# Performance work log

Hardware: AMD Instinct MI355X
Metric: run time of the kernel (lower is better)

## Reference

```python
import jax, jax.numpy as jnp
import numpy as np

B, N = 32, 512
NODE_F, EDGE_F = 64, 16
OUT = [64, 64, 64, 128]
TARGET = 16
DEGS = [1, 2, 3, 4]  # degree buckets (degree 0 filtered out, as in init_duvenaud)


def setup_inputs() -> dict:
    key = jax.random.key(0)
    ks = jax.random.split(key, 12)
    # adjacency: each node v connects to v+1..v+deg(v) (mod N), deg in {1..4}
    deg = jax.random.randint(ks[0], (B, N), 1, 5)
    off = jnp.arange(1, 5)                                   # (4,)
    cols = (jnp.arange(N)[:, None] + off[None, :]) % N       # (N,4)
    vals = (off[None, None, :] <= deg[:, :, None]).astype(jnp.float32)  # (B,N,4)
    g = jnp.zeros((B, N, N), jnp.float32).at[:, jnp.arange(N)[:, None], cols].set(vals)
    h_in = jax.random.normal(ks[1], (B, N, NODE_F), jnp.float32)
    e = jax.random.normal(ks[2], (B, N, N, EDGE_F), jnp.float32)
    # per-timestep, per-degree update matrices H_t: (n_deg, msg_in_t, out_t)
    ins = [NODE_F + EDGE_F, OUT[0] + EDGE_F, OUT[1] + EDGE_F]
    H0 = jax.random.normal(ks[3], (len(DEGS), ins[0], OUT[0]), jnp.float32)
    H1 = jax.random.normal(ks[4], (len(DEGS), ins[1], OUT[1]), jnp.float32)
    H2 = jax.random.normal(ks[5], (len(DEGS), ins[2], OUT[2]), jnp.float32)
    # readout matrices W_l for each of the 4 stored layers h^0..h^3
    layer_in = [NODE_F, OUT[0], OUT[1], OUT[2]]
    W0 = jax.random.normal(ks[6], (layer_in[0], OUT[3]), jnp.float32)
    W1 = jax.random.normal(ks[7], (layer_in[1], OUT[3]), jnp.float32)
    W2 = jax.random.normal(ks[8], (layer_in[2], OUT[3]), jnp.float32)
    W3 = jax.random.normal(ks[9], (layer_in[3], OUT[3]), jnp.float32)
    W_final = jax.random.normal(ks[10], (OUT[3], TARGET), jnp.float32) * 0.05
    b_final = jnp.zeros((TARGET,), jnp.float32)
    return {"g": g, "h_in": h_in, "e": e,
            "H0": H0, "H1": H1, "H2": H2,
            "W0": W0, "W1": W1, "W2": W2, "W3": W3,
            "W_final": W_final, "b_final": b_final}


def _step(g, e, h, H):
    # duvenaud message m_v = sum_w g[v,w] * cat(h_w, e_vw); split concat to avoid
    # materializing the (B,N,N,F+E) tensor the torch loop builds per node.
    mh = jnp.einsum('bvw,bwf->bvf', g, h)
    me = jnp.einsum('bvw,bvwe->bve', g, e)
    m = jnp.concatenate([mh, me], axis=-1)                 # (B,N,msg_in)
    deg = jnp.sum(g, axis=2)                               # (B,N) node degrees
    # degree-bucketed linear update: h'_v = m_v @ H[bucket(deg_v)]
    cand = jnp.einsum('bvm,dmo->bvdo', m, H)               # (B,N,n_deg,out)
    degs = jnp.asarray(DEGS, m.dtype)
    sel = (deg[:, :, None] == degs[None, None, :]).astype(m.dtype)  # one-hot bucket
    return jnp.einsum('bvd,bvdo->bvo', sel, cand)          # deg not in DEGS -> 0


def reference(g, h_in, e, H0, H1, H2, W0, W1, W2, W3, W_final, b_final):
    hs = [h_in]
    for H in (H0, H1, H2):
        hs.append(_step(g, e, hs[-1], H))
    # duvenaud readout: sum over layers/nodes of masked softmax(h_l @ W_l)
    acc = jnp.zeros((g.shape[0], W_final.shape[0]), h_in.dtype)
    for h, W in zip(hs, (W0, W1, W2, W3)):
        lin = jnp.einsum('bvf,fo->bvo', h, W)
        # mask rows whose linear output is all zero (padding / never-updated nodes)
        mask = (jnp.sum(lin != 0, axis=-1, keepdims=True) > 0).astype(lin.dtype)
        acc = acc + jnp.sum(jax.nn.softmax(lin, axis=-1) * mask, axis=1)
    out = acc @ W_final + b_final
    return jax.nn.softmax(out, axis=-1)
```

## Files before the change

### kernel.cpp

```cpp
#include <hip/hip_runtime.h>

#define BATCH 32
#define NN 512
#define NODE_F 64
#define EDGE_F 16
#define MSG 80
#define OUTF 64
#define RD 128
#define TGT 16
#define KMAX 8
#define ROWS (BATCH*NN)

__global__ __launch_bounds__(256) void preprocess_kernel(
    const float* __restrict__ g, const float* __restrict__ e,
    int* __restrict__ adj_idx, float* __restrict__ adj_val,
    int* __restrict__ nnzArr, int* __restrict__ bucketArr,
    float* __restrict__ me)
{
  __shared__ int   s_idx[4][KMAX];
  __shared__ float s_val[4][KMAX];
  int lane = threadIdx.x & 63;
  int wid  = threadIdx.x >> 6;
  int row  = blockIdx.x * 4 + wid;
  const float* grow = g + (size_t)row * NN;
  float deg = 0.f;
  int cnt = 0;
  for (int it = 0; it < NN/64; ++it) {
    int w = it*64 + lane;
    float gv = grow[w];
    deg += gv;
    unsigned long long m = __ballot(gv != 0.0f);
    int before = __popcll(m & ((1ull << lane) - 1ull));
    if (gv != 0.0f) {
      int pos = cnt + before;
      if (pos < KMAX) { s_idx[wid][pos] = w; s_val[wid][pos] = gv; }
    }
    cnt += __popcll(m);
  }
  for (int off = 32; off; off >>= 1) deg += __shfl_xor(deg, off);
  __syncthreads();
  const float* erow = e + (size_t)row * NN * EDGE_F;
  float mef = 0.f;
  if (cnt <= KMAX) {
    for (int k = 0; k < cnt; ++k) {
      int   wk = s_idx[wid][k];
      float vk = s_val[wid][k];
      if (lane < EDGE_F) mef += vk * erow[wk*EDGE_F + lane];
    }
  } else {
    for (int w = 0; w < NN; ++w) {
      float gv = grow[w];
      if (gv != 0.f && lane < EDGE_F) mef += gv * erow[w*EDGE_F + lane];
    }
  }
  if (lane < EDGE_F) me[(size_t)row*EDGE_F + lane] = mef;
  if (lane < KMAX && lane < cnt) {
    adj_idx[row*KMAX + lane] = s_idx[wid][lane];
    adj_val[row*KMAX + lane] = s_val[wid][lane];
  }
  if (lane == 0) {
    int bk = -1;
    if      (deg == 1.0f) bk = 0;
    else if (deg == 2.0f) bk = 1;
    else if (deg == 3.0f) bk = 2;
    else if (deg == 4.0f) bk = 3;
    bucketArr[row] = bk;
    nnzArr[row] = cnt;
  }
}

__global__ __launch_bounds__(256) void scatter_kernel(
    const int* __restrict__ bucketArr,
    int* __restrict__ counts, int* __restrict__ perm)
{
  int i = blockIdx.x * blockDim.x + threadIdx.x;
  int lane = threadIdx.x & 63;
  int bk = bucketArr[i];
  #pragma unroll
  for (int d = 0; d < 4; ++d) {
    unsigned long long m = __ballot(bk == d);
    if (m == 0ull) continue;
    int leader = __ffsll((long long)m) - 1;
    int tot    = __popcll(m);
    int base = 0;
    if (lane == leader) base = atomicAdd(&counts[d], tot);
    base = __shfl(base, leader);
    if (bk == d) {
      int before = __popcll(m & ((1ull << lane) - 1ull));
      perm[d*ROWS + base + before] = i;
    }
  }
}

__global__ __launch_bounds__(256) void step_kernel(
    const float* __restrict__ h_prev, float* __restrict__ h_out,
    const float* __restrict__ Ht,
    const int* __restrict__ perm, const int* __restrict__ counts,
    const int* __restrict__ nnzArr, const int* __restrict__ adj_idx,
    const float* __restrict__ adj_val, const float* __restrict__ me,
    const float* __restrict__ g)
{
  int d = blockIdx.x >> 8;
  int chunk = blockIdx.x & 255;
  int cnt = counts[d];
  int base = chunk * 64;
  if (base >= cnt) return;
  __shared__ float smt[MSG][68];
  __shared__ float sH[MSG*OUTF];
  __shared__ int   srow[64];
  int tid = threadIdx.x;
  int lane = tid & 63, wid = tid >> 6;
  {
    const float4* H4 = (const float4*)(Ht + (size_t)d*MSG*OUTF);
    float4* s4 = (float4*)sH;
    for (int f = tid; f < MSG*OUTF/4; f += 256) s4[f] = H4[f];
  }
  for (int t = 0; t < 16; ++t) {
    int nl = wid*16 + t;
    int gi = base + nl;
    float mh = 0.f;
    int row = -1;
    if (gi < cnt) {
      row = perm[d*ROWS + gi];
      int bb = row >> 9;
      int nnz = nnzArr[row];
      if (nnz <= KMAX) {
        for (int k = 0; k < nnz; ++k) {
          int w = adj_idx[row*KMAX + k];
          float vv = adj_val[row*KMAX + k];
          mh += vv * h_prev[((size_t)(bb*NN + w))*NODE_F + lane];
        }
      } else {
        const float* grow = g + (size_t)row * NN;
        for (int w = 0; w < NN; ++w) {
          float gv = grow[w];
          if (gv != 0.f) mh += gv * h_prev[((size_t)(bb*NN + w))*NODE_F + lane];
        }
      }
    }
    smt[lane][nl] = mh;
    if (lane < EDGE_F) smt[NODE_F + lane][nl] = (row >= 0) ? me[(size_t)row*EDGE_F + lane] : 0.f;
    if (lane == 0) srow[nl] = row;
  }
  __syncthreads();
  int tn = tid & 15, to = tid >> 4;
  float4 acc[4];
  acc[0] = acc[1] = acc[2] = acc[3] = make_float4(0.f,0.f,0.f,0.f);
  #pragma unroll 8
  for (int i = 0; i < MSG; ++i) {
    float4 hv = *(const float4*)&smt[i][4*tn];
    float4 wv = *(const float4*)&sH[i*OUTF + 4*to];
    float hk[4] = {hv.x, hv.y, hv.z, hv.w};
    #pragma unroll
    for (int k = 0; k < 4; ++k) {
      acc[k].x += hk[k]*wv.x; acc[k].y += hk[k]*wv.y;
      acc[k].z += hk[k]*wv.z; acc[k].w += hk[k]*wv.w;
    }
  }
  #pragma unroll
  for (int k = 0; k < 4; ++k) {
    int r = srow[4*tn + k];
    if (r >= 0) *(float4*)&h_out[(size_t)r*OUTF + 4*to] = acc[k];
  }
}

__global__ __launch_bounds__(256) void readout_kernel(
    const float* __restrict__ h0, const float* __restrict__ h1,
    const float* __restrict__ h2, const float* __restrict__ h3,
    const float* __restrict__ W0, const float* __restrict__ W1,
    const float* __restrict__ W2, const float* __restrict__ W3,
    float* __restrict__ accv)
{
  int l = blockIdx.x >> 8;
  int chunk = blockIdx.x & 255;
  const float* hs = (l==0)?h0:(l==1)?h1:(l==2)?h2:h3;
  const float* Wl = (l==0)?W0:(l==1)?W1:(l==2)?W2:W3;
  __shared__ float sW[NODE_F*RD];
  __shared__ float sht[NODE_F*68];
  __shared__ float snmax[64], snsum[64];
  __shared__ int   snflag[64];
  float* redm = sht;
  int*   redf = (int*)(sht + 64*17);
  int tid = threadIdx.x;
  {
    const float4* W4 = (const float4*)Wl;
    float4* sW4 = (float4*)sW;
    #pragma unroll
    for (int r = 0; r < 8; ++r) sW4[tid + 256*r] = W4[tid + 256*r];
    const float4* hv4 = (const float4*)(hs + (size_t)chunk*64*NODE_F);
    #pragma unroll
    for (int r = 0; r < 4; ++r) {
      int f = tid + 256*r;
      int n = f >> 4, c = f & 15;
      float4 v = hv4[f];
      sht[(4*c+0)*68 + n] = v.x;
      sht[(4*c+1)*68 + n] = v.y;
      sht[(4*c+2)*68 + n] = v.z;
      sht[(4*c+3)*68 + n] = v.w;
    }
  }
  __syncthreads();
  int tn = tid & 15, to = tid >> 4;
  int b = chunk >> 3;
  float4 accA[4], accB[4];
  #pragma unroll
  for (int k = 0; k < 4; ++k) { accA[k] = make_float4(0,0,0,0); accB[k] = make_float4(0,0,0,0); }
  #pragma unroll 4
  for (int i = 0; i < NODE_F; ++i) {
    float4 hv = *(const float4*)&sht[i*68 + 4*tn];
    float4 w0 = *(const float4*)&sW[i*128 + 8*to];
    float4 w1 = *(const float4*)&sW[i*128 + 8*to + 4];
    float hk[4] = {hv.x, hv.y, hv.z, hv.w};
    #pragma unroll
    for (int k = 0; k < 4; ++k) {
      accA[k].x += hk[k]*w0.x; accA[k].y += hk[k]*w0.y;
      accA[k].z += hk[k]*w0.z; accA[k].w += hk[k]*w0.w;
      accB[k].x += hk[k]*w1.x; accB[k].y += hk[k]*w1.y;
      accB[k].z += hk[k]*w1.z; accB[k].w += hk[k]*w1.w;
    }
  }
  __syncthreads();
  #pragma unroll
  for (int k = 0; k < 4; ++k) {
    float4 a = accA[k], bq = accB[k];
    float pm = fmaxf(fmaxf(fmaxf(a.x,a.y),fmaxf(a.z,a.w)),
                     fmaxf(fmaxf(bq.x,bq.y),fmaxf(bq.z,bq.w)));
    int nz = (a.x!=0.f)||(a.y!=0.f)||(a.z!=0.f)||(a.w!=0.f)||
             (bq.x!=0.f)||(bq.y!=0.f)||(bq.z!=0.f)||(bq.w!=0.f);
    int n = 4*tn + k;
    redm[n*17 + to] = pm;
    redf[n*17 + to] = nz;
  }
  __syncthreads();
  {
    int n = tid >> 2, sub = tid & 3;
    float m = redm[n*17 + sub*4 + 0];
    m = fmaxf(m, redm[n*17 + sub*4 + 1]);
    m = fmaxf(m, redm[n*17 + sub*4 + 2]);
    m = fmaxf(m, redm[n*17 + sub*4 + 3]);
    int f = redf[n*17 + sub*4 + 0] | redf[n*17 + sub*4 + 1] |
            redf[n*17 + sub*4 + 2] | redf[n*17 + sub*4 + 3];
    m = fmaxf(m, __shfl_xor(m, 1)); m = fmaxf(m, __shfl_xor(m, 2));
    f |= __shfl_xor(f, 1); f |= __shfl_xor(f, 2);
    if (sub == 0) { snmax[n] = m; snflag[n] = f; }
  }
  __syncthreads();
  #pragma unroll
  for (int k = 0; k < 4; ++k) {
    int n = 4*tn + k;
    float m = snmax[n];
    accA[k].x = __expf(accA[k].x - m); accA[k].y = __expf(accA[k].y - m);
    accA[k].z = __expf(accA[k].z - m); accA[k].w = __expf(accA[k].w - m);
    accB[k].x = __expf(accB[k].x - m); accB[k].y = __expf(accB[k].y - m);
    accB[k].z = __expf(accB[k].z - m); accB[k].w = __expf(accB[k].w - m);
    float ps = accA[k].x+accA[k].y+accA[k].z+accA[k].w+
               accB[k].x+accB[k].y+accB[k].z+accB[k].w;
    redm[n*17 + to] = ps;
  }
  __syncthreads();
  {
    int n = tid >> 2, sub = tid & 3;
    float s = redm[n*17 + sub*4 + 0] + redm[n*17 + sub*4 + 1] +
              redm[n*17 + sub*4 + 2] + redm[n*17 + sub*4 + 3];
    s += __shfl_xor(s, 1); s += __shfl_xor(s, 2);
    if (sub == 0) snsum[n] = s;
  }
  __syncthreads();
  float4 aj0 = make_float4(0,0,0,0), aj1 = make_float4(0,0,0,0);
  #pragma unroll
  for (int k = 0; k < 4; ++k) {
    int n = 4*tn + k;
    if (snflag[n]) {
      float inv = 1.0f / snsum[n];
      aj0.x += accA[k].x*inv; aj0.y += accA[k].y*inv;
      aj0.z += accA[k].z*inv; aj0.w += accA[k].w*inv;
      aj1.x += accB[k].x*inv; aj1.y += accB[k].y*inv;
      aj1.z += accB[k].z*inv; aj1.w += accB[k].w*inv;
    }
  }
  #pragma unroll
  for (int off = 1; off < 16; off <<= 1) {
    aj0.x += __shfl_xor(aj0.x, off); aj0.y += __shfl_xor(aj0.y, off);
    aj0.z += __shfl_xor(aj0.z, off); aj0.w += __shfl_xor(aj0.w, off);
    aj1.x += __shfl_xor(aj1.x, off); aj1.y += __shfl_xor(aj1.y, off);
    aj1.z += __shfl_xor(aj1.z, off); aj1.w += __shfl_xor(aj1.w, off);
  }
  if (tn == 0) {
    float* dst = &accv[b*RD + 8*to];
    atomicAdd(dst+0, aj0.x); atomicAdd(dst+1, aj0.y);
    atomicAdd(dst+2, aj0.z); atomicAdd(dst+3, aj0.w);
    atomicAdd(dst+4, aj1.x); atomicAdd(dst+5, aj1.y);
    atomicAdd(dst+6, aj1.z); atomicAdd(dst+7, aj1.w);
  }
}

__global__ __launch_bounds__(256) void final_kernel(
    const float* __restrict__ accv, const float* __restrict__ Wf,
    const float* __restrict__ bf, float* __restrict__ out)
{
  int b = blockIdx.x;
  int tid = threadIdx.x;
  int tg = tid & 15, part = tid >> 4;
  float p = 0.f;
  #pragma unroll
  for (int q = 0; q < 8; ++q) {
    int i = part*8 + q;
    p += accv[b*RD + i] * Wf[i*TGT + tg];
  }
  __shared__ float pp[16][17];
  pp[part][tg] = p;
  __syncthreads();
  if (tid < 16) {
    float v = bf[tid];
    #pragma unroll
    for (int q = 0; q < 16; ++q) v += pp[q][tid];
    float mx = v;
    for (int off = 8; off; off >>= 1) mx = fmaxf(mx, __shfl_xor(mx, off, 16));
    float e = __expf(v - mx);
    float s = e;
    for (int off = 8; off; off >>= 1) s += __shfl_xor(s, off, 16);
    out[b*TGT + tid] = e / s;
  }
}

extern "C" void kernel_launch(void* const* d_in, const int* in_sizes, int n_in,
                              void* d_out, int out_size, void* d_ws, size_t ws_size,
                              hipStream_t stream)
{
  const float* g    = (const float*)d_in[0];
  const float* h_in = (const float*)d_in[1];
  const float* e    = (const float*)d_in[2];
  const float* H0   = (const float*)d_in[3];
  const float* H1   = (const float*)d_in[4];
  const float* H2   = (const float*)d_in[5];
  const float* W0   = (const float*)d_in[6];
  const float* W1   = (const float*)d_in[7];
  const float* W2   = (const float*)d_in[8];
  const float* W3   = (const float*)d_in[9];
  const float* Wf   = (const float*)d_in[10];
  const float* bf   = (const float*)d_in[11];
  float* out = (float*)d_out;

  char* base = (char*)d_ws;
  size_t off = 0;
  auto alloc = [&](size_t bytes) -> void* {
    void* p = base + off;
    off = (off + bytes + 255) & ~(size_t)255;
    return p;
  };
  int*   adj_idx   = (int*)  alloc((size_t)ROWS*KMAX*sizeof(int));
  float* adj_val   = (float*)alloc((size_t)ROWS*KMAX*sizeof(float));
  int*   nnzArr    = (int*)  alloc((size_t)ROWS*sizeof(int));
  int*   bucketArr = (int*)  alloc((size_t)ROWS*sizeof(int));
  float* me        = (float*)alloc((size_t)ROWS*EDGE_F*sizeof(float));
  int*   perm      = (int*)  alloc((size_t)4*ROWS*sizeof(int));
  int*   counts    = (int*)  alloc(4*sizeof(int) + (size_t)BATCH*RD*sizeof(float));
  float* accv      = (float*)(counts + 4);
  float* h1        = (float*)alloc((size_t)ROWS*NODE_F*sizeof(float)*3);
  float* h2 = h1 + (size_t)ROWS*NODE_F;
  float* h3 = h2 + (size_t)ROWS*NODE_F;

  hipMemsetAsync(counts, 0, 4*sizeof(int) + (size_t)BATCH*RD*sizeof(float), stream);
  hipMemsetAsync(h1, 0, (size_t)ROWS*NODE_F*sizeof(float)*3, stream);

  preprocess_kernel<<<ROWS/4, 256, 0, stream>>>(g, e, adj_idx, adj_val, nnzArr, bucketArr, me);
  scatter_kernel<<<ROWS/256, 256, 0, stream>>>(bucketArr, counts, perm);
  step_kernel<<<4*256, 256, 0, stream>>>(h_in, h1, H0, perm, counts, nnzArr, adj_idx, adj_val, me, g);
  step_kernel<<<4*256, 256, 0, stream>>>(h1,   h2, H1, perm, counts, nnzArr, adj_idx, adj_val, me, g);
  step_kernel<<<4*256, 256, 0, stream>>>(h2,   h3, H2, perm, counts, nnzArr, adj_idx, adj_val, me, g);
  readout_kernel<<<4*256, 256, 0, stream>>>(h_in, h1, h2, h3, W0, W1, W2, W3, accv);
  final_kernel<<<BATCH, 256, 0, stream>>>(accv, Wf, bf, out);
}
```

Measured before the change: 787.4 us.

## Fold memsets into preprocess, parallelize edge gather, vectorize adjacency loads

Drops the two hipMemsetAsync calls. The preprocess kernel now zeroes the accumulator and counts itself, and writes zeros to h1..h3 only for rows with no valid degree bucket. The edge-feature gather now spreads the up to 8 neighbours across all 64 lanes and reduces with shuffles, where before it ran a serial loop on 16 lanes. The step kernel reads adjacency indices and values as int4/float4 and unrolls the neighbour loop. The risk is correctness if any h row outside the buckets is left unwritten.

```diff
diff --git a/kernel.cpp b/kernel.cpp
--- a/kernel.cpp
+++ b/kernel.cpp
@@ -15,12 +15,18 @@
     const float* __restrict__ g, const float* __restrict__ e,
     int* __restrict__ adj_idx, float* __restrict__ adj_val,
     int* __restrict__ nnzArr, int* __restrict__ bucketArr,
-    float* __restrict__ me)
+    float* __restrict__ me,
+    float* __restrict__ h1, float* __restrict__ h2, float* __restrict__ h3,
+    float* __restrict__ accv, int* __restrict__ counts)
 {
   __shared__ int   s_idx[4][KMAX];
   __shared__ float s_val[4][KMAX];
-  int lane = threadIdx.x & 63;
-  int wid  = threadIdx.x >> 6;
+  int tid  = threadIdx.x;
+  int gtid = blockIdx.x * 256 + tid;
+  if (gtid < BATCH*RD) accv[gtid] = 0.f;
+  if (gtid < 4) counts[gtid] = 0;
+  int lane = tid & 63;
+  int wid  = tid >> 6;
   int row  = blockIdx.x * 4 + wid;
   const float* grow = g + (size_t)row * NN;
   float deg = 0.f;
@@ -40,30 +46,40 @@
   for (int off = 32; off; off >>= 1) deg += __shfl_xor(deg, off);
   __syncthreads();
   const float* erow = e + (size_t)row * NN * EDGE_F;
-  float mef = 0.f;
   if (cnt <= KMAX) {
-    for (int k = 0; k < cnt; ++k) {
-      int   wk = s_idx[wid][k];
-      float vk = s_val[wid][k];
-      if (lane < EDGE_F) mef += vk * erow[wk*EDGE_F + lane];
-    }
+    int k = lane >> 4, f = lane & 15;
+    float part = 0.f;
+    if (k < cnt)     part  = s_val[wid][k]   * erow[s_idx[wid][k]  *EDGE_F + f];
+    if (cnt > 4) {
+      int k2 = k + 4;
+      if (k2 < cnt)  part += s_val[wid][k2]  * erow[s_idx[wid][k2] *EDGE_F + f];
+    }
+    part += __shfl_xor(part, 32);
+    part += __shfl_xor(part, 16);
+    if (lane < EDGE_F) me[(size_t)row*EDGE_F + lane] = part;
   } else {
+    float mef = 0.f;
     for (int w = 0; w < NN; ++w) {
       float gv = grow[w];
       if (gv != 0.f && lane < EDGE_F) mef += gv * erow[w*EDGE_F + lane];
     }
-  }
-  if (lane < EDGE_F) me[(size_t)row*EDGE_F + lane] = mef;
+    if (lane < EDGE_F) me[(size_t)row*EDGE_F + lane] = mef;
+  }
   if (lane < KMAX && lane < cnt) {
     adj_idx[row*KMAX + lane] = s_idx[wid][lane];
     adj_val[row*KMAX + lane] = s_val[wid][lane];
   }
+  int bk = -1;
+  if      (deg == 1.0f) bk = 0;
+  else if (deg == 2.0f) bk = 1;
+  else if (deg == 3.0f) bk = 2;
+  else if (deg == 4.0f) bk = 3;
+  if (bk < 0) {
+    h1[(size_t)row*NODE_F + lane] = 0.f;
+    h2[(size_t)row*NODE_F + lane] = 0.f;
+    h3[(size_t)row*NODE_F + lane] = 0.f;
+  }
   if (lane == 0) {
-    int bk = -1;
-    if      (deg == 1.0f) bk = 0;
-    else if (deg == 2.0f) bk = 1;
-    else if (deg == 3.0f) bk = 2;
-    else if (deg == 4.0f) bk = 3;
     bucketArr[row] = bk;
     nnzArr[row] = cnt;
   }
@@ -115,6 +131,7 @@
     float4* s4 = (float4*)sH;
     for (int f = tid; f < MSG*OUTF/4; f += 256) s4[f] = H4[f];
   }
+  #pragma unroll 2
   for (int t = 0; t < 16; ++t) {
     int nl = wid*16 + t;
     int gi = base + nl;
@@ -125,10 +142,20 @@
       int bb = row >> 9;
       int nnz = nnzArr[row];
       if (nnz <= KMAX) {
-        for (int k = 0; k < nnz; ++k) {
-          int w = adj_idx[row*KMAX + k];
-          float vv = adj_val[row*KMAX + k];
-          mh += vv * h_prev[((size_t)(bb*NN + w))*NODE_F + lane];
+        int4   ai = *(const int4*)  &adj_idx[row*KMAX];
+        float4 av = *(const float4*)&adj_val[row*KMAX];
+        const float* hb = h_prev + (size_t)bb*NN*NODE_F + lane;
+        if (nnz > 0) mh += av.x * hb[(size_t)ai.x*NODE_F];
+        if (nnz > 1) mh += av.y * hb[(size_t)ai.y*NODE_F];
+        if (nnz > 2) mh += av.z * hb[(size_t)ai.z*NODE_F];
+        if (nnz > 3) mh += av.w * hb[(size_t)ai.w*NODE_F];
+        if (nnz > 4) {
+          int4   ai2 = *(const int4*)  &adj_idx[row*KMAX + 4];
+          float4 av2 = *(const float4*)&adj_val[row*KMAX + 4];
+          mh += av2.x * hb[(size_t)ai2.x*NODE_F];
+          if (nnz > 5) mh += av2.y * hb[(size_t)ai2.y*NODE_F];
+          if (nnz > 6) mh += av2.z * hb[(size_t)ai2.z*NODE_F];
+          if (nnz > 7) mh += av2.w * hb[(size_t)ai2.w*NODE_F];
         }
       } else {
         const float* grow = g + (size_t)row * NN;
@@ -360,10 +387,8 @@
   float* h2 = h1 + (size_t)ROWS*NODE_F;
   float* h3 = h2 + (size_t)ROWS*NODE_F;
 
-  hipMemsetAsync(counts, 0, 4*sizeof(int) + (size_t)BATCH*RD*sizeof(float), stream);
-  hipMemsetAsync(h1, 0, (size_t)ROWS*NODE_F*sizeof(float)*3, stream);
-
-  preprocess_kernel<<<ROWS/4, 256, 0, stream>>>(g, e, adj_idx, adj_val, nnzArr, bucketArr, me);
+  preprocess_kernel<<<ROWS/4, 256, 0, stream>>>(g, e, adj_idx, adj_val, nnzArr, bucketArr, me,
+                                                h1, h2, h3, accv, counts);
   scatter_kernel<<<ROWS/256, 256, 0, stream>>>(bucketArr, counts, perm);
   step_kernel<<<4*256, 256, 0, stream>>>(h_in, h1, H0, perm, counts, nnzArr, adj_idx, adj_val, me, g);
   step_kernel<<<4*256, 256, 0, stream>>>(h1,   h2, H1, perm, counts, nnzArr, adj_idx, adj_val, me, g);
```

Measured after the change: 770.5 us. -2.1%, faster.
